# Optimization experiments

Hardware: AMD Instinct MI355X
Metric: run time of the kernel (lower is better)

Reference implementation:

```python
import jax, jax.numpy as jnp
import numpy as np

T_, N_, NL, E_ = 32, 64, 64, 128
VOCAB, NTOK = 128, 4
D_, HW, K_, STRIDE, PAD, CH = 16, 16, 3, 1, 1, 64
INVN, RH, PAVOC, NPA, LE = 32, 64, 32, 4, 64
HD, A_, NE = 512, 16, 4


def setup_inputs():
    key = jax.random.key(0)
    ks = jax.random.split(key, 32)
    s = 0.05
    rn = lambda i, shp: jax.random.normal(ks[i], shp, jnp.float32)
    return dict(
        lines=jax.random.randint(ks[0], (N_, NL, NTOK), 0, VOCAB),
        obs=rn(1, (T_, N_, D_, HW, HW)),
        inventory=rn(2, (T_, N_, INVN)),
        partial_action=jax.random.randint(ks[3], (T_, N_, NPA), 0, PAVOC),
        action_mask=(jax.random.uniform(ks[4], (T_, N_, A_)) > 0.2).astype(jnp.float32),
        p0=jnp.zeros((N_,), jnp.int32),
        emb_task=rn(5, (VOCAB, E_)) * s,
        emb_lower=rn(6, (PAVOC, LE)) * s,
        gru_wi_f=rn(7, (3 * E_, E_)) * s, gru_wh_f=rn(8, (3 * E_, E_)) * s,
        gru_bi_f=jnp.zeros((3 * E_,)), gru_bh_f=jnp.zeros((3 * E_,)),
        gru_wi_b=rn(9, (3 * E_, E_)) * s, gru_wh_b=rn(10, (3 * E_, E_)) * s,
        gru_bi_b=jnp.zeros((3 * E_,)), gru_bh_b=jnp.zeros((3 * E_,)),
        beta_w=rn(11, (E_, NE)) * s, beta_b=jnp.zeros((NE,)),
        kernel_w=rn(12, (E_, CH * D_ * K_ * K_)) * s, kernel_b=jnp.zeros((CH * D_ * K_ * K_,)),
        conv_bias=jnp.zeros((CH,)),
        inv_w=rn(13, (INVN, RH)) * s, inv_b=jnp.zeros((RH,)),
        zeta1_w=rn(14, (E_ + CH + RH + LE, HD)) * s, zeta1_b=jnp.zeros((HD,)),
        actor_w=rn(15, (HD, A_)) * s, actor_b=jnp.zeros((A_,)),
        upsilon_w=rn(16, (E_ + CH + RH + LE, NE)) * s, upsilon_b=jnp.zeros((NE,)),
        dgate_w=rn(17, (E_ + CH + RH + LE, 2)) * s, dgate_b=jnp.zeros((2,)),
        critic_w=rn(18, (HD, 1)) * s, critic_b=jnp.zeros((1,)),
    )


def _gru_dir(x, wi, wh, bi, bh):
    # unidirectional GRU over axis 1; torch gate order (r, z, n)
    def step(h, xt):
        gi = xt @ wi.T + bi
        gh = h @ wh.T + bh
        ir, iz, inn = jnp.split(gi, 3, axis=-1)
        hr, hz, hn = jnp.split(gh, 3, axis=-1)
        r = jax.nn.sigmoid(ir + hr)
        z = jax.nn.sigmoid(iz + hz)
        n = jnp.tanh(inn + r * hn)
        h = (1.0 - z) * n + z * h
        return h, h
    h0 = jnp.zeros((x.shape[0], wi.shape[1]), x.dtype)
    _, hs = jax.lax.scan(step, h0, jnp.swapaxes(x, 0, 1))
    return jnp.swapaxes(hs, 0, 1)


def _forward(lines, obs, inventory, partial_action, action_mask, p0, emb_task, emb_lower,
             gru_wi_f, gru_wh_f, gru_bi_f, gru_bh_f, gru_wi_b, gru_wh_b, gru_bi_b, gru_bh_b,
             beta_w, beta_b, kernel_w, kernel_b, conv_bias, inv_w, inv_b, zeta1_w, zeta1_b,
             actor_w, actor_b, upsilon_w, upsilon_b, dgate_w, dgate_b, critic_w, critic_b):
    N, nl = lines.shape[0], lines.shape[1]
    dt = obs.dtype
    # MultiEmbeddingBag: sum token embeddings per line -> M [N, nl, E]
    M = emb_task[lines].sum(axis=2)
    # all cyclic rolls of M, as in torch.stack([roll(M,-i,1) for i in range(nl)]) -> [nl, N, nl, E]
    shift = (jnp.arange(nl)[:, None] + jnp.arange(nl)[None, :]) % nl
    rolled = jnp.transpose(M[:, shift], (1, 0, 2, 3))
    R = jnp.arange(N)
    last = jnp.zeros((1, 2 * nl, 1), dt).at[:, -1, :].set(1.0)
    old = jax.nn.one_hot(jnp.full((N,), nl), 2 * nl, dtype=dt)  # delta=0 one-hot

    def step_t(p, xs):
        obs_t, inv_t, pa_t, amask_t = xs
        x = rolled[p, R]                                   # [N, nl, E] per-example roll by pointer
        fwd = _gru_dir(x, gru_wi_f, gru_wh_f, gru_bi_f, gru_bh_f)
        bwd = _gru_dir(x[:, ::-1], gru_wi_b, gru_wh_b, gru_bi_b, gru_bh_b)[:, ::-1]
        G = jnp.stack([fwd, bwd], axis=2)                  # [N, nl, 2, E]
        B = jax.nn.sigmoid(G @ beta_w + beta_b)            # [N, nl, 2, NE]
        B = jnp.stack([B[:, :, 0], B[:, :, 1][:, ::-1]], axis=2).reshape(N, 2 * nl, NE)
        B = (1.0 - last)[:, ::-1] * B
        zero_last = (1.0 - last) * B
        B = zero_last + last
        C = jnp.cumprod(1.0 - jnp.roll(zero_last, 1, axis=1), axis=1)
        P = (B * C).reshape(N, nl, 2, NE)
        P = jnp.concatenate([P[:, :, 1][:, ::-1], P[:, :, 0]], axis=1)  # [N, 2nl, NE]
        m = M[R, p]                                        # [N, E]
        kern = (m @ kernel_w + kernel_b).reshape(N, CH, D_, K_, K_)
        conv1 = lambda o, w: jax.lax.conv_general_dilated(o[None], w, (STRIDE, STRIDE), [(PAD, PAD), (PAD, PAD)])[0]
        h1 = jax.vmap(conv1)(obs_t, kern) + conv_bias[None, :, None, None]
        h1 = jax.nn.relu(h1).sum((-2, -1))                 # [N, CH]
        inv = jax.nn.relu(inv_t @ inv_w + inv_b)
        pa = emb_lower[pa_t].sum(axis=1)                   # embedding-bag sum
        z_in = jnp.concatenate([m, h1, inv, pa], axis=-1)
        z1 = jax.nn.relu(z_in @ zeta1_w + zeta1_b)
        a_probs = jax.nn.softmax(z1 @ actor_w + actor_b, axis=-1) * amask_t
        u = jax.nn.softmax(z_in @ upsilon_w + upsilon_b, axis=-1)
        d_probs = jnp.einsum('nle,ne->nl', P, u)
        dg_probs = jax.nn.softmax(z_in @ dgate_w + dgate_b, axis=-1)
        dg = jnp.argmax(dg_probs, axis=-1)
        g = dg.astype(dt)[:, None]
        dsel = jnp.argmax(g * d_probs + (1.0 - g) * old, axis=-1)  # gate() with argmax action
        a = jnp.argmax(a_probs, axis=-1)
        v = z1 @ critic_w + critic_b
        p_new = jnp.clip(p + dsel.astype(p.dtype) - nl, 0, nl - 1)
        out = jnp.concatenate([a[:, None].astype(dt), a_probs, dsel[:, None].astype(dt), d_probs,
                               z1, p_new[:, None].astype(dt), v, dg_probs, dg[:, None].astype(dt)], axis=-1)
        return p_new, out

    _, outs = jax.lax.scan(step_t, p0, (obs, inventory, partial_action, action_mask))
    return outs  # [T, N, 1+A+1+2nl+HD+1+1+2+1]


def reference(lines, obs, inventory, partial_action, action_mask, p0, emb_task, emb_lower,
              gru_wi_f, gru_wh_f, gru_bi_f, gru_bh_f, gru_wi_b, gru_wh_b, gru_bi_b, gru_bh_b,
              beta_w, beta_b, kernel_w, kernel_b, conv_bias, inv_w, inv_b, zeta1_w, zeta1_b,
              actor_w, actor_b, upsilon_w, upsilon_b, dgate_w, dgate_b, critic_w, critic_b):
    return _forward(lines, obs, inventory, partial_action, action_mask, p0, emb_task, emb_lower,
                    gru_wi_f, gru_wh_f, gru_bi_f, gru_bh_f, gru_wi_b, gru_wh_b, gru_bi_b, gru_bh_b,
                    beta_w, beta_b, kernel_w, kernel_b, conv_bias, inv_w, inv_b, zeta1_w, zeta1_b,
                    actor_w, actor_b, upsilon_w, upsilon_b, dgate_w, dgate_b, critic_w, critic_b)
```

## Files before the change

kernel.cpp:

```cpp
#include <hip/hip_runtime.h>
#include <math.h>

#define T_   32
#define N_   64
#define NL   64
#define E_   128
#define G3   384
#define NE   4
#define CH   64
#define D_   16
#define HW   16
#define RH   64
#define LE   64
#define HD   512
#define A_   16
#define INVN 32
#define KCOLS 9216
#define OUTW 663
#define OXP  24
#define OROW 456
#define OPL  8664
#define KPITCH 168

typedef _Float16 half8 __attribute__((ext_vector_type(8)));
typedef _Float16 half4 __attribute__((ext_vector_type(4)));
typedef float floatx4 __attribute__((ext_vector_type(4)));

__device__ __forceinline__ float fsig(float x)  { return __builtin_amdgcn_rcpf(1.f + __expf(-x)); }
__device__ __forceinline__ float ftanh(float x) { return 1.f - 2.f*__builtin_amdgcn_rcpf(1.f + __expf(2.f*x)); }

__global__ __launch_bounds__(256) void k_prep1(
    const int* lines, const float* emb_task, float* M,
    const float* wif, const float* wib, float* wiT4,
    const float* whf, const float* whb, _Float16* WBpack,
    const float* inv, const float* inv_w, const float* inv_b,
    const int* pa, const float* emb_lower, float* inv_all, float* pa_all,
    int* flags, const float* kernel_w, float* kernel_wpT) {
    int b = blockIdx.x, tid = threadIdx.x;
    __shared__ float Tt[128][149];
    if (b < 1024) {
        #pragma unroll
        for (int r = 0; r < 2; ++r) {
            int idx = b*512 + r*256 + tid;
            int nl = idx >> 7, i = idx & 127;
            const int* ln = lines + nl*4;
            float s = 0.f;
            #pragma unroll
            for (int t = 0; t < 4; ++t) s += emb_task[ln[t]*E_ + i];
            M[nl*E_ + i] = s;
        }
    } else if (b < 1408) {
        int ob = (b - 1024)*2 + (tid >> 7);
        int g = ob % 384, dir = ob / 384;
        int k = tid & 127;
        const float* wi = dir ? wib : wif;
        int dst = ((dir*32 + (k>>2))*384 + g)*4 + (k&3);
        wiT4[dst] = wi[g*128 + k];
    } else if (b < 1504) {
        int ob = (b - 1408)*4 + (tid >> 6);
        int lane = tid & 63;
        int nt = ob % 6; int rest = ob / 6;
        int term = rest % 2; rest /= 2;
        int kt = rest % 4; rest /= 4;
        int w = rest % 4; int dir = rest / 4;
        const float* wh = dir ? whb : whf;
        int gt = nt >> 1, isub = nt & 1;
        int g  = gt*128 + w*32 + isub*16 + (lane & 15);
        int k0 = kt*32 + (lane >> 4)*8;
        _Float16* dst = WBpack + (size_t)ob*512 + lane*8;
        #pragma unroll
        for (int e = 0; e < 8; ++e) {
            float v = wh[g*128 + k0 + e];
            _Float16 hi = (_Float16)v;
            dst[e] = (term == 0) ? hi : (_Float16)(v - (float)hi);
        }
    } else if (b < 2016) {
        int tn = (b - 1504)*4 + (tid >> 6);
        int r = tid & 63;
        const float* iv = inv + tn*INVN;
        float acc = inv_b[r];
        #pragma unroll
        for (int i = 0; i < INVN; ++i) acc += iv[i]*inv_w[i*RH + r];
        inv_all[tn*RH + r] = fmaxf(acc, 0.f);
        const int* pp = pa + tn*4;
        float s = 0.f;
        #pragma unroll
        for (int j = 0; j < 4; ++j) s += emb_lower[pp[j]*LE + r];
        pa_all[tn*LE + r] = s;
    } else if (b < 2161) {
        int idx = (b - 2016)*256 + tid;
        if (idx < 36992) flags[idx] = 0;
    } else {
        int c = b - 2161;
        for (int idx = tid; idx < 128*144; idx += 256) {
            int r = idx / 144, q = idx - r*144;
            Tt[r][q] = kernel_w[(size_t)r*KCOLS + c*144 + q];
        }
        __syncthreads();
        for (int idx = tid; idx < 144*128; idx += 256) {
            int cl = idx >> 7, k = idx & 127;
            int ta = cl >> 4, d = cl & 15;
            kernel_wpT[(size_t)(c*144 + cl)*E_ + k] = Tt[k][d*9 + ta];
        }
    }
}

__global__ __launch_bounds__(256) void k_mid(
    const float* M, const float* inv_all, const float* pa_all,
    const float* zw, const float* zb,
    const float* uw, const float* ub, const float* dw, const float* db,
    const int* p0, int* p_arr, int* pflag,
    float* zmp, float* zip, float* ump, float* dmp, float* uip, float* dip,
    const float* kernel_wpT, const float* kernel_b, unsigned int* kernu,
    const float* wiT4, const float* bif, const float* bib, float* giM) {
    int b = blockIdx.x, tid = threadIdx.x;
    if (b < 481) {
        if (b < 256) {
            int cb = b & 1, rb = b >> 1;
            __shared__ float At[32][E_];
            for (int idx = tid; idx < 32*E_; idx += 256) {
                int r = idx >> 7, k = idx & 127;
                At[r][k] = M[(rb*32 + r)*E_ + k];
            }
            __syncthreads();
            float acc[32];
            #pragma unroll
            for (int r = 0; r < 32; ++r) acc[r] = 0.f;
            int col = cb*256 + tid;
            #pragma unroll 4
            for (int k = 0; k < E_; ++k) {
                float w = zw[k*HD + col];
                #pragma unroll
                for (int r = 0; r < 32; ++r) acc[r] += At[r][k]*w;
            }
            #pragma unroll
            for (int r = 0; r < 32; ++r)
                zmp[(size_t)(rb*32 + r)*HD + col] = acc[r];
        } else if (b < 384) {
            int b2 = b - 256;
            int cb = b2 & 1, rb = b2 >> 1;
            __shared__ float At2[32][E_];
            for (int idx = tid; idx < 32*E_; idx += 256) {
                int r = idx >> 7, k = idx & 127;
                int row = rb*32 + r;
                At2[r][k] = (k < 64) ? inv_all[row*RH + k] : pa_all[row*LE + (k - 64)];
            }
            __syncthreads();
            float acc[32];
            #pragma unroll
            for (int r = 0; r < 32; ++r) acc[r] = 0.f;
            int col = cb*256 + tid;
            #pragma unroll 4
            for (int k = 0; k < E_; ++k) {
                float w = zw[(192 + k)*HD + col];
                #pragma unroll
                for (int r = 0; r < 32; ++r) acc[r] += At2[r][k]*w;
            }
            float bb = zb[col];
            #pragma unroll
            for (int r = 0; r < 32; ++r)
                zip[(size_t)(rb*32 + r)*HD + col] = acc[r] + bb;
        } else if (b < 448) {
            int wg = b - 384;
            __shared__ float Mt[64][E_];
            for (int idx = tid; idx < 64*E_; idx += 256)
                ((float*)Mt)[idx] = M[(size_t)wg*64*E_ + idx];
            __syncthreads();
            int r = tid >> 2, q = tid & 3;
            float au = 0.f, ad = 0.f;
            #pragma unroll 4
            for (int k = 0; k < E_; ++k) {
                float m = Mt[r][k];
                au += m*uw[k*NE + q];
                if (q < 2) ad += m*dw[k*2 + q];
            }
            int row = wg*64 + r;
            ump[row*NE + q] = au;
            if (q < 2) dmp[row*2 + q] = ad;
        } else if (b < 480) {
            int wg = b - 448;
            __shared__ float At3[64][E_];
            for (int idx = tid; idx < 64*E_; idx += 256) {
                int r = idx >> 7, k = idx & 127;
                int row = wg*64 + r;
                At3[r][k] = (k < 64) ? inv_all[row*RH + k] : pa_all[row*LE + (k - 64)];
            }
            __syncthreads();
            int r = tid >> 2, q = tid & 3;
            float au = ub[q], ad = (q < 2) ? db[q] : 0.f;
            #pragma unroll 4
            for (int k = 0; k < E_; ++k) {
                float v = At3[r][k];
                au += v*uw[(192 + k)*NE + q];
                if (q < 2) ad += v*dw[(192 + k)*2 + q];
            }
            int row = wg*64 + r;
            uip[row*NE + q] = au;
            if (q < 2) dip[row*2 + q] = ad;
        } else {
            if (tid < 64) {
                p_arr[tid] = p0[tid];
                pflag[tid] = 1;
            }
        }
    } else if (b < 2785) {
        int bb = b - 481;
        int cb = bb % 72, rb = bb / 72;
        int lane = tid & 63, wv = tid >> 6;
        int quad = lane >> 4, xl = lane & 15;

        __shared__ _Float16 Ah[128*40], Al[128*40];
        __shared__ _Float16 Bh[128*40], Bl[128*40];

        floatx4 a0[2][8], a1[2][8];
        #pragma unroll
        for (int rt = 0; rt < 2; ++rt)
            #pragma unroll
            for (int ct = 0; ct < 8; ++ct) {
                a0[rt][ct] = (floatx4){0.f,0.f,0.f,0.f};
                a1[rt][ct] = (floatx4){0.f,0.f,0.f,0.f};
            }

        for (int kc = 0; kc < 4; ++kc) {
            #pragma unroll
            for (int l = 0; l < 4; ++l) {
                int idx = tid + l*256;
                int r = idx >> 3, kq = idx & 7;
                float4 v = *(const float4*)&M[(size_t)(rb*128 + r)*E_ + kc*32 + kq*4];
                half4 hv, lv;
                hv.x=(_Float16)v.x; lv.x=(_Float16)((v.x-(float)hv.x)*1024.f);
                hv.y=(_Float16)v.y; lv.y=(_Float16)((v.y-(float)hv.y)*1024.f);
                hv.z=(_Float16)v.z; lv.z=(_Float16)((v.z-(float)hv.z)*1024.f);
                hv.w=(_Float16)v.w; lv.w=(_Float16)((v.w-(float)hv.w)*1024.f);
                *(half4*)&Ah[r*40 + kq*4] = hv;
                *(half4*)&Al[r*40 + kq*4] = lv;
            }
            #pragma unroll
            for (int l = 0; l < 4; ++l) {
                int idx = tid + l*256;
                int c = idx >> 3, kq = idx & 7;
                float4 v = *(const float4*)&kernel_wpT[(size_t)(cb*128 + c)*E_ + kc*32 + kq*4];
                half4 hv, lv;
                hv.x=(_Float16)v.x; lv.x=(_Float16)((v.x-(float)hv.x)*1024.f);
                hv.y=(_Float16)v.y; lv.y=(_Float16)((v.y-(float)hv.y)*1024.f);
                hv.z=(_Float16)v.z; lv.z=(_Float16)((v.z-(float)hv.z)*1024.f);
                hv.w=(_Float16)v.w; lv.w=(_Float16)((v.w-(float)hv.w)*1024.f);
                *(half4*)&Bh[c*40 + kq*4] = hv;
                *(half4*)&Bl[c*40 + kq*4] = lv;
            }
            __syncthreads();
            half8 ah[2], al[2];
            #pragma unroll
            for (int rt = 0; rt < 2; ++rt) {
                int m = wv*32 + rt*16 + xl;
                ah[rt] = *(const half8*)&Ah[m*40 + quad*8];
                al[rt] = *(const half8*)&Al[m*40 + quad*8];
            }
            #pragma unroll
            for (int ct = 0; ct < 8; ++ct) {
                int c = ct*16 + xl;
                half8 bh = *(const half8*)&Bh[c*40 + quad*8];
                half8 bl = *(const half8*)&Bl[c*40 + quad*8];
                #pragma unroll
                for (int rt = 0; rt < 2; ++rt) {
                    a0[rt][ct] = __builtin_amdgcn_mfma_f32_16x16x32_f16(ah[rt], bh, a0[rt][ct], 0,0,0);
                    a1[rt][ct] = __builtin_amdgcn_mfma_f32_16x16x32_f16(al[rt], bh, a1[rt][ct], 0,0,0);
                    a1[rt][ct] = __builtin_amdgcn_mfma_f32_16x16x32_f16(ah[rt], bl, a1[rt][ct], 0,0,0);
                }
            }
            __syncthreads();
        }
        #pragma unroll
        for (int ct = 0; ct < 8; ++ct) {
            int colp = cb*128 + ct*16 + xl;
            int c = colp / 144, rr = colp % 144;
            int ta = rr >> 4, d = rr & 15;
            float kb = kernel_b[c*144 + d*9 + ta];
            #pragma unroll
            for (int rt = 0; rt < 2; ++rt)
                #pragma unroll
                for (int r = 0; r < 4; ++r) {
                    float v = a0[rt][ct][r] + a1[rt][ct][r]*(1.f/1024.f) + kb;
                    _Float16 h = (_Float16)v;
                    _Float16 lo = (_Float16)((v - (float)h)*1024.f);
                    union { _Float16 f; unsigned short u; } H, L;
                    H.f = h; L.f = lo;
                    size_t row = (size_t)rb*128 + wv*32 + rt*16 + quad*4 + r;
                    kernu[row*(size_t)KCOLS + colp] = ((unsigned)L.u << 16) | (unsigned)H.u;
                }
        }
    } else {
        int ob = b - 2785;
        int lblk = ob & 7, n = (ob >> 3) & 63, dir = ob >> 9;
        __shared__ float Ml[8][E_];
        for (int idx = tid; idx < 8*E_; idx += 256) {
            int r = idx >> 7, k = idx & 127;
            Ml[r][k] = M[(n*NL + lblk*8 + r)*E_ + k];
        }
        __syncthreads();
        const float4* W = (const float4*)(wiT4) + dir*32*384;
        for (int g = tid; g < 384; g += 256) {
            float acc[8];
            #pragma unroll
            for (int r = 0; r < 8; ++r) acc[r] = 0.f;
            for (int kq = 0; kq < 32; ++kq) {
                float4 w = W[kq*384 + g];
                #pragma unroll
                for (int r = 0; r < 8; ++r) {
                    float4 h = *(const float4*)&Ml[r][kq*4];
                    acc[r] += w.x*h.x + w.y*h.y + w.z*h.z + w.w*h.w;
                }
            }
            float bi = dir ? bib[g] : bif[g];
            #pragma unroll
            for (int r = 0; r < 8; ++r)
                giM[((dir*N_ + n)*NL + lblk*8 + r)*G3 + g] = acc[r] + bi;
        }
    }
}

__global__ __launch_bounds__(256, 2) void k_gru(const float* giM, const _Float16* WBpack,
                                                const float* bhf, const float* bhb,
                                                const float* beta_w, const float* beta_b,
                                                float* Ball) {
    int b = blockIdx.x;
    int x = b & 7, m = b >> 3;
    int pblk = m & 3;
    int s = x + 8*(m >> 2);
    int dir = s >> 6, n = s & 63;
    int tid = threadIdx.x;
    int w = tid >> 6;
    int lane = tid & 63;
    int quad = lane >> 4;
    int col  = lane & 15;

    __shared__ _Float16 Hhi[16*136];
    __shared__ _Float16 Hlo[16*136];
    __shared__ float    Hf[16*132];
    __shared__ float    bwT[4*132];
    __shared__ float    giR[32][G3];
    for (int idx = tid; idx < 16*136; idx += 256) { Hhi[idx] = (_Float16)0.f; Hlo[idx] = (_Float16)0.f; }
    for (int idx = tid; idx < 16*132; idx += 256) Hf[idx] = 0.f;
    for (int idx = tid; idx < 512; idx += 256) { int k = idx >> 2, e = idx & 3; bwT[e*132 + k] = beta_w[k*NE + e]; }

    half8 WB[48];
    const half8* wsrc = (const half8*)(WBpack) + ((size_t)(dir*4 + w)*4)*12*64;
    #pragma unroll
    for (int f = 0; f < 48; ++f) WB[f] = wsrc[(size_t)f*64 + lane];

    const float* bh = dir ? bhb : bhf;
    float bhv[6];
    #pragma unroll
    for (int gt2 = 0; gt2 < 3; ++gt2) {
        bhv[gt2*2+0] = bh[gt2*128 + w*32 + col];
        bhv[gt2*2+1] = bh[gt2*128 + w*32 + col + 16];
    }
    const float* giBase = giM + (size_t)(dir*N_ + n)*NL*G3;

    {
        int start0 = dir ? ((pblk*16 + 63) & 63) : (pblk*16 & 63);
        for (int idx = tid; idx < 16*G3; idx += 256) {
            int sr = idx / G3, e = idx - sr*G3;
            int l = (start0 + sr) & 63;
            giR[l & 31][e] = giBase[(size_t)l*G3 + e];
        }
    }

    int bseq = tid >> 4, bsub = tid & 15, bee = bsub & 3, bpart = bsub >> 2;
    float bbias = beta_b[bee];
    __syncthreads();

    for (int j = 0; j < NL; ++j) {
        floatx4 C[6];
        #pragma unroll
        for (int reg = 0; reg < 4; ++reg) {
            int seq = quad*4 + reg;
            int p = pblk*16 + seq;
            int l = dir ? ((p + 63 - j) & 63) : ((p + j) & 63);
            const float* gl = &giR[l & 31][w*32 + col];
            #pragma unroll
            for (int gt2 = 0; gt2 < 2; ++gt2)
                #pragma unroll
                for (int isub = 0; isub < 2; ++isub)
                    C[gt2*2 + isub][reg] = gl[gt2*128 + isub*16] + bhv[gt2*2+isub];
            #pragma unroll
            for (int isub = 0; isub < 2; ++isub)
                C[4 + isub][reg] = bhv[4+isub];
        }
        #pragma unroll
        for (int kt = 0; kt < 4; ++kt) {
            int off = col*136 + kt*32 + quad*8;
            half8 ahi = *(const half8*)&Hhi[off];
            half8 alo = *(const half8*)&Hlo[off];
            #pragma unroll
            for (int nt = 0; nt < 6; ++nt) {
                half8 bhi2 = WB[kt*12 + nt];
                half8 blo2 = WB[kt*12 + 6 + nt];
                C[nt] = __builtin_amdgcn_mfma_f32_16x16x32_f16(ahi, bhi2, C[nt], 0,0,0);
                C[nt] = __builtin_amdgcn_mfma_f32_16x16x32_f16(alo, bhi2, C[nt], 0,0,0);
                C[nt] = __builtin_amdgcn_mfma_f32_16x16x32_f16(ahi, blo2, C[nt], 0,0,0);
            }
        }
        __syncthreads();

        if (j < 63) {
            int lnext = dir ? ((pblk*16 + 62 - j) & 63) : ((pblk*16 + j + 16) & 63);
            for (int idx = tid; idx < G3; idx += 256)
                giR[lnext & 31][idx] = giBase[(size_t)lnext*G3 + idx];
        }

        #pragma unroll
        for (int reg = 0; reg < 4; ++reg) {
            int seq = quad*4 + reg;
            int p = pblk*16 + seq;
            int l = dir ? ((p + 63 - j) & 63) : ((p + j) & 63);
            const float* gl2 = &giR[l & 31][256 + w*32 + col];
            #pragma unroll
            for (int isub = 0; isub < 2; ++isub) {
                int i = w*32 + isub*16 + col;
                float r  = fsig(C[isub][reg]);
                float z  = fsig(C[2 + isub][reg]);
                float nn = ftanh(gl2[isub*16] + r*C[4 + isub][reg]);
                float hold = Hf[seq*132 + i];
                float hnew = (1.f - z)*nn + z*hold;
                _Float16 hi = (_Float16)hnew;
                _Float16 lo = (_Float16)(hnew - (float)hi);
                Hf[seq*132 + i] = hnew;
                Hhi[seq*136 + i] = hi;
                Hlo[seq*136 + i] = lo;
            }
        }
        __syncthreads();

        {
            float acc = 0.f;
            const float* hrow = &Hf[bseq*132];
            const float* brow = &bwT[bee*132];
            #pragma unroll 8
            for (int kk = 0; kk < 32; ++kk) {
                int k2 = bpart + 4*kk;
                acc += hrow[k2]*brow[k2];
            }
            acc += __shfl_xor(acc, 4);
            acc += __shfl_xor(acc, 8);
            if (bpart == 0) {
                float bval = fsig(acc + bbias);
                int p = pblk*16 + bseq;
                Ball[((n*NL + p)*128 + 2*j + dir)*NE + bee] = bval;
            }
        }
    }
}

__global__ __launch_bounds__(448, 1) void k_step(
    const float* obs, const unsigned int* kernu, const float* conv_bias,
    const float* zmp, const float* zip,
    const float* ump, const float* uip, const float* dmp, const float* dip,
    const float* zw, const float* aw, const float* ab,
    const float* uw, const float* dw, const float* cw, const float* cb,
    const float* amask, const float* Ball, const int* p0,
    float* out) {

    int n = blockIdx.x, tid = threadIdx.x;

    __shared__ __align__(16) _Float16 obs_h[2][OPL];
    __shared__ __align__(16) _Float16 obs_lo[2][OPL];
    __shared__ __align__(16) _Float16 klh[64*KPITCH];
    __shared__ __align__(16) _Float16 kll[64*KPITCH];
    __shared__ float h1part[4][64];
    __shared__ __align__(16) float zml[2][HD];
    __shared__ __align__(16) float zil[2][HD];
    __shared__ __align__(16) float Pl[HD];
    __shared__ __align__(16) float Btmp[HD];
    __shared__ __align__(16) float aml[2][16];
    __shared__ __align__(16) float uws[CH*NE];
    __shared__ __align__(16) float dws[CH*2];
    __shared__ float cbl[CH];
    __shared__ __align__(16) float umpl[4];
    __shared__ __align__(16) float uipl[4];
    __shared__ __align__(8)  float dmpl[2];
    __shared__ __align__(8)  float dipl[2];
    __shared__ float h1l[2][CH];
    __shared__ __align__(16) float z1l[HD];
    __shared__ float pla[128];
    __shared__ float pc[32];
    __shared__ float la[A_];
    __shared__ float lu[4];
    __shared__ float ld2[2];
    __shared__ float scv[1];
    __shared__ int   psint[2];

    int lane = tid & 63;
    int wv   = tid >> 6;
    int quad = lane >> 4;
    int xl   = lane & 15;

    auto stage_kern = [&](int prow) {
        if (tid < 256) {
            const uint4* src = (const uint4*)(kernu + (size_t)(n*NL + prow)*KCOLS);
            #pragma unroll
            for (int l = 0; l < 9; ++l) {
                int i = tid + l*256;
                uint4 v = src[i];
                int e = i*4;
                int c = e / 144, k = e - c*144;
                union { unsigned short u[4]; half4 h; } H, L;
                H.u[0] = (unsigned short)(v.x & 0xffffu); L.u[0] = (unsigned short)(v.x >> 16);
                H.u[1] = (unsigned short)(v.y & 0xffffu); L.u[1] = (unsigned short)(v.y >> 16);
                H.u[2] = (unsigned short)(v.z & 0xffffu); L.u[2] = (unsigned short)(v.z >> 16);
                H.u[3] = (unsigned short)(v.w & 0xffffu); L.u[3] = (unsigned short)(v.w >> 16);
                *(half4*)&klh[c*KPITCH + k] = H.h;
                *(half4*)&kll[c*KPITCH + k] = L.h;
            }
        }
    };

    auto tail_partA = [&](int tt, int bpar) {
        int w45 = (tid - 256) >> 6;
        int ln  = tid & 63;
        size_t ob2 = ((size_t)tt*N_ + n)*OUTW;
        #pragma unroll
        for (int c8i = 0; c8i < 4; ++c8i) {
            int c8 = w45*4 + c8i;
            int h = c8*64 + ln;
            float a2 = zml[bpar][h] + zil[bpar][h];
            #pragma unroll 16
            for (int cc = 0; cc < CH; ++cc) a2 += h1l[bpar][cc]*zw[(E_ + cc)*HD + h];
            float v = fmaxf(a2, 0.f);
            z1l[h] = v;
            out[ob2 + 146 + h] = v;
        }
        {
            int a3 = ln & 15, part = (ln >> 4) + w45*4;
            float acc2 = 0.f;
            const float* z0 = z1l + part*64;
            #pragma unroll 16
            for (int h = 0; h < 64; ++h) acc2 += z0[h]*aw[(part*64 + h)*A_ + a3];
            pla[a3*8 + part] = acc2;
        }
        if (ln < 16) {
            int e = w45*16 + ln;
            float acc2 = 0.f;
            const float* z0 = z1l + e*16;
            #pragma unroll 16
            for (int h = 0; h < 16; ++h) acc2 += z0[h]*cw[e*16 + h];
            pc[e] = acc2;
        }
    };

    auto tail_partB = [&](int tt, int bpar) {
        int ln = tid - 256;
        size_t ob2 = ((size_t)tt*N_ + n)*OUTW;
        if (ln < A_) {
            float acc2 = ab[ln];
            #pragma unroll
            for (int k = 0; k < 8; ++k) acc2 += pla[ln*8 + k];
            la[ln] = acc2;
        } else if (ln == 24) {
            float acc2 = cb[0];
            #pragma unroll
            for (int k = 0; k < 32; ++k) acc2 += pc[k];
            scv[0] = acc2;
        }
        if (ln == 0) {
            float mx = la[0];
            #pragma unroll
            for (int k2 = 1; k2 < A_; ++k2) mx = fmaxf(mx, la[k2]);
            float pr[A_]; float sum = 0.f;
            #pragma unroll
            for (int k2 = 0; k2 < A_; ++k2) { pr[k2] = expf(la[k2]-mx); sum += pr[k2]; }
            const float* am = &aml[bpar][0];
            float best = -1.f; int bi2 = 0;
            #pragma unroll
            for (int k2 = 0; k2 < A_; ++k2) {
                float v = pr[k2]/sum * am[k2];
                out[ob2 + 1 + k2] = v;
                if (v > best) { best = v; bi2 = k2; }
            }
            out[ob2 + 0] = (float)bi2;
        } else if (ln == 1) {
            out[ob2 + 659] = scv[0];
        }
    };

    int pcur = p0[n];
    {
        if (tid == 0) psint[1] = pcur;
        for (int i = tid; i < OPL; i += 448) {
            obs_h[0][i] = (_Float16)0.f; obs_h[1][i] = (_Float16)0.f;
            obs_lo[0][i] = (_Float16)0.f; obs_lo[1][i] = (_Float16)0.f;
        }
        for (int i = tid; i < 64*(KPITCH-144); i += 448) {
            int c = i / (KPITCH-144), k = 144 + i % (KPITCH-144);
            klh[c*KPITCH + k] = (_Float16)0.f;
            kll[c*KPITCH + k] = (_Float16)0.f;
        }
        if (tid < 64) cbl[tid] = conv_bias[tid];
        if (tid < 256) {
            uws[tid] = uw[(E_ + (tid >> 2))*NE + (tid & 3)];
            if (tid < 128) dws[tid] = dw[(E_ + (tid >> 1))*2 + (tid & 1)];
        }
    }
    __syncthreads();
    {
        if (tid < 256) {
            const float4* op4 = (const float4*)(obs + (size_t)(0*N_ + n)*D_*HW*HW);
            #pragma unroll
            for (int k4 = 0; k4 < 4; ++k4) {
                int idx = tid + k4*256;
                float4 v = op4[idx];
                int d = idx >> 6, rem = idx & 63;
                int y = rem >> 2, xq = rem & 3;
                int base = (y+1)*OROW + (xq*4+1)*OXP + d;
                _Float16 h0=(_Float16)v.x, h1=(_Float16)v.y, h2=(_Float16)v.z, h3=(_Float16)v.w;
                obs_h[0][base+0*OXP] = h0; obs_lo[0][base+0*OXP] = (_Float16)((v.x-(float)h0)*1024.f);
                obs_h[0][base+1*OXP] = h1; obs_lo[0][base+1*OXP] = (_Float16)((v.y-(float)h1)*1024.f);
                obs_h[0][base+2*OXP] = h2; obs_lo[0][base+2*OXP] = (_Float16)((v.z-(float)h2)*1024.f);
                obs_h[0][base+3*OXP] = h3; obs_lo[0][base+3*OXP] = (_Float16)((v.w-(float)h3)*1024.f);
            }
        }
        stage_kern(pcur);
    }
    __syncthreads();

    for (int t = 0; t < T_; ++t) {
        int par = t & 1;
        size_t ob = ((size_t)t*N_ + n)*OUTW;

        if (tid < 256) {
            floatx4 a0[4][4];
            floatx4 a1[4][4];
            #pragma unroll
            for (int jm = 0; jm < 4; ++jm)
                #pragma unroll
                for (int ct = 0; ct < 4; ++ct) {
                    a0[jm][ct] = (floatx4){0.f,0.f,0.f,0.f};
                    a1[jm][ct] = (floatx4){0.f,0.f,0.f,0.f};
                }
            const _Float16* Oh = &obs_h[par][0];
            const _Float16* Ol = &obs_lo[par][0];
            #pragma unroll
            for (int kt = 0; kt < 5; ++kt) {
                int pi = kt*2 + (quad >> 1);
                int ky = (pi*11) >> 5;
                int kx = pi - ky*3;
                int aoff = ky*OROW + kx*OXP + ((quad & 1) << 3) + xl*OXP;
                half8 ah[4], al[4];
                #pragma unroll
                for (int jm = 0; jm < 4; ++jm) {
                    int y = wv*4 + jm;
                    int o = aoff + y*OROW;
                    ah[jm] = *(const half8*)&Oh[o];
                    al[jm] = *(const half8*)&Ol[o];
                }
                #pragma unroll
                for (int ct = 0; ct < 4; ++ct) {
                    int bo = (ct*16 + xl)*KPITCH + kt*32 + quad*8;
                    half8 bh = *(const half8*)&klh[bo];
                    half8 bl = *(const half8*)&kll[bo];
                    #pragma unroll
                    for (int jm = 0; jm < 4; ++jm) {
                        a0[jm][ct] = __builtin_amdgcn_mfma_f32_16x16x32_f16(ah[jm], bh, a0[jm][ct], 0,0,0);
                        a1[jm][ct] = __builtin_amdgcn_mfma_f32_16x16x32_f16(al[jm], bh, a1[jm][ct], 0,0,0);
                        a1[jm][ct] = __builtin_amdgcn_mfma_f32_16x16x32_f16(ah[jm], bl, a1[jm][ct], 0,0,0);
                    }
                }
            }
            #pragma unroll
            for (int ct = 0; ct < 4; ++ct) {
                float bc = cbl[ct*16 + xl];
                float s = 0.f;
                #pragma unroll
                for (int jm = 0; jm < 4; ++jm) {
                    float sj = 0.f;
                    #pragma unroll
                    for (int r = 0; r < 4; ++r)
                        sj += fmaxf(a0[jm][ct][r] + a1[jm][ct][r]*(1.f/1024.f) + bc, 0.f);
                    s += sj;
                }
                s += __shfl_xor(s, 16);
                s += __shfl_xor(s, 32);
                if (quad == 0) h1part[wv][ct*16 + xl] = s;
            }
        } else if (tid < 384) {
            if (t > 0) tail_partA(t - 1, 1 - par);
        } else {
            int ln5 = tid - 384;
            int pp = psint[1];
            const float4* Brow = (const float4*)(Ball + (size_t)(n*NL + pp)*128*NE);
            const float4* Zm   = (const float4*)(zmp  + (size_t)(n*NL + pp)*HD);
            const float4* Zi   = (const float4*)(zip  + (size_t)(t*N_ + n)*HD);
            #pragma unroll
            for (int k = 0; k < 2; ++k) {
                ((float4*)Btmp)[k*64 + ln5]         = Brow[k*64 + ln5];
                ((float4*)&zml[par][0])[k*64 + ln5] = Zm[k*64 + ln5];
                ((float4*)&zil[par][0])[k*64 + ln5] = Zi[k*64 + ln5];
            }
            if (ln5 < 4) {
                ((float4*)&aml[par][0])[ln5] = ((const float4*)(amask + ((size_t)t*N_ + n)*A_))[ln5];
            } else if (ln5 == 4) {
                *(float4*)umpl = *(const float4*)(ump + (size_t)(n*NL + pp)*NE);
            } else if (ln5 == 5) {
                *(float4*)uipl = *(const float4*)(uip + (size_t)(t*N_ + n)*NE);
            } else if (ln5 == 6) {
                *(float2*)dmpl = *(const float2*)(dmp + (size_t)(n*NL + pp)*2);
            } else if (ln5 == 7) {
                *(float2*)dipl = *(const float2*)(dip + (size_t)(t*N_ + n)*2);
            }
            if (ln5 < NE) {
                int e = ln5;
                float c = 1.f;
                for (int j2 = 0; j2 < 128; ++j2) {
                    float bzv = (j2 == 0 || j2 == 127) ? 0.f : Btmp[j2*NE + e];
                    float bf = (j2 == 127) ? 1.f : bzv;
                    float pf = bf * c;
                    c *= (1.f - bzv);
                    int j = (j2 & 1) ? (63 - ((j2 - 1) >> 1)) : ((j2 >> 1) + 64);
                    Pl[j*NE + e] = pf;
                }
            }
            if (t + 1 < T_) {
                const float4* op4 = (const float4*)(obs + (size_t)((t+1)*N_ + n)*D_*HW*HW);
                _Float16* dh = &obs_h[1 - par][0];
                _Float16* dl = &obs_lo[1 - par][0];
                #pragma unroll
                for (int k4 = 0; k4 < 16; ++k4) {
                    int idx = k4*64 + ln5;
                    float4 v = op4[idx];
                    int d = idx >> 6, rem = idx & 63;
                    int y = rem >> 2, xq = rem & 3;
                    int base = (y+1)*OROW + (xq*4+1)*OXP + d;
                    _Float16 h0=(_Float16)v.x, h1=(_Float16)v.y, h2=(_Float16)v.z, h3=(_Float16)v.w;
                    dh[base+0*OXP] = h0; dl[base+0*OXP] = (_Float16)((v.x-(float)h0)*1024.f);
                    dh[base+1*OXP] = h1; dl[base+1*OXP] = (_Float16)((v.y-(float)h1)*1024.f);
                    dh[base+2*OXP] = h2; dl[base+2*OXP] = (_Float16)((v.z-(float)h2)*1024.f);
                    dh[base+3*OXP] = h3; dl[base+3*OXP] = (_Float16)((v.w-(float)h3)*1024.f);
                }
            }
        }
        __syncthreads();

        if (wv < 4) {
            float hp = ((h1part[0][lane] + h1part[1][lane]) + h1part[2][lane]) + h1part[3][lane];
            h1l[par][lane] = hp;
            if (lane < 4) {
                float a2 = umpl[lane] + uipl[lane];
                #pragma unroll 16
                for (int cc = 0; cc < CH; ++cc) a2 += h1l[par][cc]*uws[cc*4 + lane];
                lu[lane] = a2;
            } else if (lane < 6) {
                int g = lane - 4;
                float a2 = dmpl[g] + dipl[g];
                #pragma unroll 16
                for (int cc = 0; cc < CH; ++cc) a2 += h1l[par][cc]*dws[cc*2 + g];
                ld2[g] = a2;
            }
            float l0 = lu[0], l1 = lu[1], l2 = lu[2], l3 = lu[3];
            float d0 = ld2[0], d1 = ld2[1];
            float mx = fmaxf(fmaxf(l0, l1), fmaxf(l2, l3));
            float e0u = expf(l0-mx), e1u = expf(l1-mx), e2u = expf(l2-mx), e3u = expf(l3-mx);
            float su = ((e0u + e1u) + e2u) + e3u;
            float uv0 = e0u/su, uv1 = e1u/su, uv2 = e2u/su, uv3 = e3u/su;
            int dg = (d1 > d0) ? 1 : 0;

            float4 Pva = ((const float4*)Pl)[lane];
            float4 Pvb = ((const float4*)Pl)[lane + 64];
            float va = Pva.x*uv0 + Pva.y*uv1 + Pva.z*uv2 + Pva.w*uv3;
            float vb = Pvb.x*uv0 + Pvb.y*uv1 + Pvb.z*uv2 + Pvb.w*uv3;
            if (tid < 64) {
                out[ob + 18 + lane] = va;
                out[ob + 82 + lane] = vb;
            }
            float bv = va; int bj = lane;
            if (vb > va) { bv = vb; bj = lane + 64; }
            #pragma unroll
            for (int off2 = 1; off2 < 64; off2 <<= 1) {
                float v2 = __shfl_xor(bv, off2);
                int   j2 = __shfl_xor(bj, off2);
                if (v2 > bv || (v2 == bv && j2 < bj)) { bv = v2; bj = j2; }
            }
            int dsel = dg ? bj : 64;
            int pn = pcur + dsel - 64;
            pn = pn < 0 ? 0 : (pn > 63 ? 63 : pn);
            if (tid == 0) {
                out[ob + 17]  = (float)dsel;
                out[ob + 658] = (float)pn;
                psint[1] = pn;
            } else if (tid == 2) {
                float mx2 = fmaxf(d0, d1);
                float q0 = expf(d0-mx2), q1 = expf(d1-mx2);
                float s2 = q0 + q1;
                out[ob + 660] = q0/s2;
                out[ob + 661] = q1/s2;
                out[ob + 662] = (float)dg;
            }
            if (t + 1 < T_ && pn != pcur) stage_kern(pn);
            pcur = pn;
        } else if (wv == 4) {
            if (t > 0) tail_partB(t - 1, 1 - par);
        }
        __syncthreads();
    }

    if (tid >= 256 && tid < 384) tail_partA(T_ - 1, 1);
    __syncthreads();
    if (wv == 4) tail_partB(T_ - 1, 1);
}

extern "C" void kernel_launch(void* const* d_in, const int* in_sizes, int n_in,
                              void* d_out, int out_size, void* d_ws, size_t ws_size,
                              hipStream_t stream) {
    (void)in_sizes; (void)n_in; (void)out_size; (void)ws_size;
    const int*   lines    = (const int*)  d_in[0];
    const float* obs      = (const float*)d_in[1];
    const float* invent   = (const float*)d_in[2];
    const int*   pa       = (const int*)  d_in[3];
    const float* amask    = (const float*)d_in[4];
    const int*   p0       = (const int*)  d_in[5];
    const float* emb_task = (const float*)d_in[6];
    const float* emb_low  = (const float*)d_in[7];
    const float* wi_f     = (const float*)d_in[8];
    const float* wh_f     = (const float*)d_in[9];
    const float* bi_f     = (const float*)d_in[10];
    const float* bh_f     = (const float*)d_in[11];
    const float* wi_b     = (const float*)d_in[12];
    const float* wh_b     = (const float*)d_in[13];
    const float* bi_b     = (const float*)d_in[14];
    const float* bh_b     = (const float*)d_in[15];
    const float* beta_w   = (const float*)d_in[16];
    const float* beta_b   = (const float*)d_in[17];
    const float* kernel_w = (const float*)d_in[18];
    const float* kernel_b = (const float*)d_in[19];
    const float* conv_b   = (const float*)d_in[20];
    const float* inv_w    = (const float*)d_in[21];
    const float* inv_b    = (const float*)d_in[22];
    const float* zw       = (const float*)d_in[23];
    const float* zb       = (const float*)d_in[24];
    const float* aw       = (const float*)d_in[25];
    const float* ab       = (const float*)d_in[26];
    const float* uw       = (const float*)d_in[27];
    const float* ub       = (const float*)d_in[28];
    const float* dw       = (const float*)d_in[29];
    const float* db       = (const float*)d_in[30];
    const float* cw       = (const float*)d_in[31];
    const float* cb       = (const float*)d_in[32];
    float* out = (float*)d_out;

    float* ws = (float*)d_ws;
    size_t off = 0;
    float* M        = ws + off; off += (size_t)N_*NL*E_;
    float* wiT4     = ws + off; off += 2*32*384*4;
    _Float16* WBpack = (_Float16*)(ws + off); off += (size_t)384*512/2;
    float* giM      = ws + off; off += (size_t)2*N_*NL*G3;
    float* Ball     = ws + off; off += (size_t)N_*NL*128*NE;
    float* Pall     = ws + off; off += (size_t)N_*NL*128*NE;
    float* inv_all  = ws + off; off += (size_t)T_*N_*RH;
    float* pa_all   = ws + off; off += (size_t)T_*N_*LE;
    unsigned int* kernu = (unsigned int*)(ws + off); off += (size_t)N_*NL*KCOLS;
    float* h1_buf   = ws + off; off += (size_t)T_*N_*64;
    float* zmp      = ws + off; off += (size_t)N_*NL*HD;
    float* zip      = ws + off; off += (size_t)T_*N_*HD;
    float* ump      = ws + off; off += (size_t)N_*NL*NE;
    float* dmp      = ws + off; off += (size_t)N_*NL*2;
    float* uip      = ws + off; off += (size_t)T_*N_*NE;
    float* dip      = ws + off; off += (size_t)T_*N_*2;
    int*   flags    = (int*)(ws + off); off += 36992;
    int*   pflag    = flags + 32768;
    int*   p_arr    = pflag + 2112;
    float* kernel_wpT = ws + off; off += (size_t)E_*KCOLS;
    (void)h1_buf; (void)Pall;

    k_prep1<<<2225, 256, 0, stream>>>(lines, emb_task, M, wi_f, wi_b, wiT4,
                                      wh_f, wh_b, WBpack,
                                      invent, inv_w, inv_b, pa, emb_low, inv_all, pa_all,
                                      flags, kernel_w, kernel_wpT);
    k_mid<<<3809, 256, 0, stream>>>(M, inv_all, pa_all, zw, zb, uw, ub, dw, db,
                                    p0, p_arr, pflag,
                                    zmp, zip, ump, dmp, uip, dip,
                                    kernel_wpT, kernel_b, kernu,
                                    wiT4, bi_f, bi_b, giM);
    k_gru<<<512, 256, 0, stream>>>(giM, WBpack, bh_f, bh_b, beta_w, beta_b, Ball);

    k_step<<<64, 448, 0, stream>>>(obs, kernu, conv_b,
                                   zmp, zip, ump, uip, dmp, dip,
                                   zw, aw, ab, uw, dw, cw, cb,
                                   amask, Ball, p0, out);
}
```

Before: 1.271 ms.

## Rebalance k_step wave roles: add a wave, move obs staging to tail waves

Raises the k_step block size from 448 to 512 threads, giving 8 waves. Wave 4 now only does the beam/P computation, and waves 5-7 run tail_partA (work split 3/3/2). The next-step obs staging moves from wave 4's first phase into waves 5-7's second phase, where they were idle. The aim is to shorten the critical path of the first phase of each timestep, at the cost of more register pressure from the larger block and a reworked work split that may be uneven.

```diff
diff --git a/kernel.cpp b/kernel.cpp
--- a/kernel.cpp
+++ b/kernel.cpp
@@ -452,7 +452,7 @@
     }
 }
 
-__global__ __launch_bounds__(448, 1) void k_step(
+__global__ __launch_bounds__(512, 1) void k_step(
     const float* obs, const unsigned int* kernu, const float* conv_bias,
     const float* zmp, const float* zip,
     const float* ump, const float* uip, const float* dmp, const float* dip,
@@ -516,12 +516,13 @@
     };
 
     auto tail_partA = [&](int tt, int bpar) {
-        int w45 = (tid - 256) >> 6;
-        int ln  = tid & 63;
+        int w57 = wv - 5;
+        int ln  = lane;
         size_t ob2 = ((size_t)tt*N_ + n)*OUTW;
-        #pragma unroll
-        for (int c8i = 0; c8i < 4; ++c8i) {
-            int c8 = w45*4 + c8i;
+        int c8start = w57*3;
+        int c8cnt = (w57 < 2) ? 3 : 2;
+        for (int c8i = 0; c8i < c8cnt; ++c8i) {
+            int c8 = c8start + c8i;
             int h = c8*64 + ln;
             float a2 = zml[bpar][h] + zil[bpar][h];
             #pragma unroll 16
@@ -530,16 +531,19 @@
             z1l[h] = v;
             out[ob2 + 146 + h] = v;
         }
-        {
-            int a3 = ln & 15, part = (ln >> 4) + w45*4;
+        int nparts = (w57 < 2) ? 3 : 2;
+        if (ln < nparts*16) {
+            int a3 = ln & 15, part = w57*3 + (ln >> 4);
             float acc2 = 0.f;
             const float* z0 = z1l + part*64;
             #pragma unroll 16
             for (int h = 0; h < 64; ++h) acc2 += z0[h]*aw[(part*64 + h)*A_ + a3];
             pla[a3*8 + part] = acc2;
         }
-        if (ln < 16) {
-            int e = w45*16 + ln;
+        int pcStart = w57*11;
+        int pcCnt = (w57 == 2) ? 10 : 11;
+        if (ln >= 48 && ln < 48 + pcCnt) {
+            int e = pcStart + (ln - 48);
             float acc2 = 0.f;
             const float* z0 = z1l + e*16;
             #pragma unroll 16
@@ -549,7 +553,7 @@
     };
 
     auto tail_partB = [&](int tt, int bpar) {
-        int ln = tid - 256;
+        int ln = lane;
         size_t ob2 = ((size_t)tt*N_ + n)*OUTW;
         if (ln < A_) {
             float acc2 = ab[ln];
@@ -583,14 +587,35 @@
         }
     };
 
+    auto stage_obs = [&](int tnext, int par_next) {
+        int w57 = wv - 5;
+        const float4* op4 = (const float4*)(obs + (size_t)(tnext*N_ + n)*D_*HW*HW);
+        _Float16* dh = &obs_h[par_next][0];
+        _Float16* dl = &obs_lo[par_next][0];
+        for (int j = 0; j < 6; ++j) {
+            int idx = j*192 + w57*64 + lane;
+            if (idx < 1024) {
+                float4 v = op4[idx];
+                int d = idx >> 6, rem = idx & 63;
+                int y = rem >> 2, xq = rem & 3;
+                int base = (y+1)*OROW + (xq*4+1)*OXP + d;
+                _Float16 h0=(_Float16)v.x, h1=(_Float16)v.y, h2=(_Float16)v.z, h3=(_Float16)v.w;
+                dh[base+0*OXP] = h0; dl[base+0*OXP] = (_Float16)((v.x-(float)h0)*1024.f);
+                dh[base+1*OXP] = h1; dl[base+1*OXP] = (_Float16)((v.y-(float)h1)*1024.f);
+                dh[base+2*OXP] = h2; dl[base+2*OXP] = (_Float16)((v.z-(float)h2)*1024.f);
+                dh[base+3*OXP] = h3; dl[base+3*OXP] = (_Float16)((v.w-(float)h3)*1024.f);
+            }
+        }
+    };
+
     int pcur = p0[n];
     {
         if (tid == 0) psint[1] = pcur;
-        for (int i = tid; i < OPL; i += 448) {
+        for (int i = tid; i < OPL; i += 512) {
             obs_h[0][i] = (_Float16)0.f; obs_h[1][i] = (_Float16)0.f;
             obs_lo[0][i] = (_Float16)0.f; obs_lo[1][i] = (_Float16)0.f;
         }
-        for (int i = tid; i < 64*(KPITCH-144); i += 448) {
+        for (int i = tid; i < 64*(KPITCH-144); i += 512) {
             int c = i / (KPITCH-144), k = 144 + i % (KPITCH-144);
             klh[c*KPITCH + k] = (_Float16)0.f;
             kll[c*KPITCH + k] = (_Float16)0.f;
@@ -627,7 +652,7 @@
         int par = t & 1;
         size_t ob = ((size_t)t*N_ + n)*OUTW;
 
-        if (tid < 256) {
+        if (wv < 4) {
             floatx4 a0[4][4];
             floatx4 a1[4][4];
             #pragma unroll
@@ -682,10 +707,8 @@
                 s += __shfl_xor(s, 32);
                 if (quad == 0) h1part[wv][ct*16 + xl] = s;
             }
-        } else if (tid < 384) {
-            if (t > 0) tail_partA(t - 1, 1 - par);
-        } else {
-            int ln5 = tid - 384;
+        } else if (wv == 4) {
+            int ln5 = lane;
             int pp = psint[1];
             const float4* Brow = (const float4*)(Ball + (size_t)(n*NL + pp)*128*NE);
             const float4* Zm   = (const float4*)(zmp  + (size_t)(n*NL + pp)*HD);
@@ -719,24 +742,8 @@
                     Pl[j*NE + e] = pf;
                 }
             }
-            if (t + 1 < T_) {
-                const float4* op4 = (const float4*)(obs + (size_t)((t+1)*N_ + n)*D_*HW*HW);
-                _Float16* dh = &obs_h[1 - par][0];
-                _Float16* dl = &obs_lo[1 - par][0];
-                #pragma unroll
-                for (int k4 = 0; k4 < 16; ++k4) {
-                    int idx = k4*64 + ln5;
-                    float4 v = op4[idx];
-                    int d = idx >> 6, rem = idx & 63;
-                    int y = rem >> 2, xq = rem & 3;
-                    int base = (y+1)*OROW + (xq*4+1)*OXP + d;
-                    _Float16 h0=(_Float16)v.x, h1=(_Float16)v.y, h2=(_Float16)v.z, h3=(_Float16)v.w;
-                    dh[base+0*OXP] = h0; dl[base+0*OXP] = (_Float16)((v.x-(float)h0)*1024.f);
-                    dh[base+1*OXP] = h1; dl[base+1*OXP] = (_Float16)((v.y-(float)h1)*1024.f);
-                    dh[base+2*OXP] = h2; dl[base+2*OXP] = (_Float16)((v.z-(float)h2)*1024.f);
-                    dh[base+3*OXP] = h3; dl[base+3*OXP] = (_Float16)((v.w-(float)h3)*1024.f);
-                }
-            }
+        } else {
+            if (t > 0) tail_partA(t - 1, 1 - par);
         }
         __syncthreads();
 
@@ -798,11 +805,13 @@
             pcur = pn;
         } else if (wv == 4) {
             if (t > 0) tail_partB(t - 1, 1 - par);
+        } else {
+            if (t + 1 < T_) stage_obs(t + 1, 1 - par);
         }
         __syncthreads();
     }
 
-    if (tid >= 256 && tid < 384) tail_partA(T_ - 1, 1);
+    if (wv >= 5) tail_partA(T_ - 1, 1);
     __syncthreads();
     if (wv == 4) tail_partB(T_ - 1, 1);
 }
@@ -881,7 +890,7 @@
                                     wiT4, bi_f, bi_b, giM);
     k_gru<<<512, 256, 0, stream>>>(giM, WBpack, bh_f, bh_b, beta_w, beta_b, Ball);
 
-    k_step<<<64, 448, 0, stream>>>(obs, kernu, conv_b,
+    k_step<<<64, 512, 0, stream>>>(obs, kernu, conv_b,
                                    zmp, zip, ump, uip, dmp, dip,
                                    zw, aw, ab, uw, dw, cw, cb,
                                    amask, Ball, p0, out);
```

Result: faster. 1.138 ms (-10.5%).
